# Performance work log

Hardware: AMD Instinct MI355X
Metric: run time of the kernel (lower is better)

The kernel has to match this reference:

```python
import jax, jax.numpy as jnp
import numpy as np

EPS = 1e-5

def _segment_mean(src_feat, edge_index, num_targets):
    # src_feat: [Ns, D]; edge_index: [2, E] = [source_idx, target_idx]
    msgs = src_feat[edge_index[0]]                                   # [E, D] gather
    agg = jax.ops.segment_sum(msgs, edge_index[1], num_segments=num_targets)
    deg = jax.ops.segment_sum(jnp.ones((edge_index.shape[1],), src_feat.dtype),
                              edge_index[1], num_segments=num_targets)
    return agg / jnp.clip(deg, 1.0)[:, None]

def _layernorm(x, gamma, beta):
    mu = jnp.mean(x, axis=-1, keepdims=True)
    var = jnp.mean(jnp.square(x - mu), axis=-1, keepdims=True)
    return (x - mu) * jax.lax.rsqrt(var + EPS) * gamma + beta

def setup_inputs() -> dict:
    key = jax.random.key(0)
    ks = jax.random.split(key, 8)
    NU, NI, E, D = 50000, 50000, 300000, 256
    s = 1.0 / np.sqrt(D)
    return {
        "user_features": jax.random.normal(ks[0], (NU, D), jnp.float32),
        "item_features": jax.random.normal(ks[1], (NI, D), jnp.float32),
        "user_item_edge_index": jax.random.randint(ks[2], (2, E), 0, NI),
        "item_user_edge_index": jax.random.randint(ks[3], (2, E), 0, NU),
        "Wu": jax.random.uniform(ks[4], (D, D), jnp.float32, -s, s),
        "bu": jax.random.uniform(ks[5], (D,), jnp.float32, -s, s),
        "Wi": jax.random.uniform(ks[6], (D, D), jnp.float32, -s, s),
        "bi": jax.random.uniform(ks[7], (D,), jnp.float32, -s, s),
        "gamma": jnp.ones((D,), jnp.float32),
        "beta": jnp.zeros((D,), jnp.float32),
    }

def reference(user_features, item_features, user_item_edge_index, item_user_edge_index,
              Wu, bu, Wi, bi, gamma, beta):
    num_items = item_features.shape[0]
    num_users = user_features.shape[0]
    # messages into items come from users; into users come from items
    item_messages = _segment_mean(user_features, user_item_edge_index, num_items)
    user_messages = _segment_mean(item_features, item_user_edge_index, num_users)
    u_new = (user_features + user_messages) @ Wu + bu
    i_new = (item_features + item_messages) @ Wi + bi
    u_new = _layernorm(jax.nn.relu(u_new), gamma, beta)
    i_new = _layernorm(jax.nn.relu(i_new), gamma, beta)
    return (u_new, i_new)
```

## Files before the change

kernel.cpp:

```cpp
#include <hip/hip_runtime.h>
#include <hip/hip_bf16.h>

#define D 256
#define BM 64
#define LDA 264
#define LDAF 260
#define LDK 72

typedef __attribute__((ext_vector_type(8))) __bf16 bf16x8;
typedef __attribute__((ext_vector_type(4))) float f32x4;

__device__ __forceinline__ float bf2f(unsigned short u) {
    union { unsigned int i; float f; } c; c.i = ((unsigned int)u) << 16; return c.f;
}
__device__ __forceinline__ float bf2f_lo(unsigned int u) {
    union { unsigned int i; float f; } c; c.i = u << 16; return c.f;
}
__device__ __forceinline__ float bf2f_hi(unsigned int u) {
    union { unsigned int i; float f; } c; c.i = u & 0xffff0000u; return c.f;
}
__device__ __forceinline__ unsigned short f2bf(float f) {
    __hip_bfloat16 h = __float2bfloat16(f);
    return *reinterpret_cast<unsigned short*>(&h);
}
__device__ __forceinline__ unsigned int pack2(float lo, float hi) {
    return (unsigned int)f2bf(lo) | ((unsigned int)f2bf(hi) << 16);
}


__global__ void k_prep(const float* __restrict__ uf, const float* __restrict__ itf,
                       const float* __restrict__ Wu, const float* __restrict__ Wi,
                       unsigned short* __restrict__ feat_bf,
                       unsigned short* __restrict__ Wt_u, unsigned short* __restrict__ Wt_i,
                       const int* __restrict__ iu_e, int Eiu,
                       const int* __restrict__ ui_e, int Eui,
                       int* __restrict__ deg, int NU,
                       size_t nfU, size_t nfTot, int nbF) {
    int b = blockIdx.x;
    if (b < nbF) {
        size_t base = ((size_t)b * 256 + threadIdx.x) * 8;
        if (base < nfTot) {
            const float* s = (base < nfU) ? (uf + base) : (itf + (base - nfU));
            float4 f0 = *(const float4*)s;
            float4 f1 = *(const float4*)(s + 4);
            ushort4 o0, o1;
            o0.x = f2bf(f0.x); o0.y = f2bf(f0.y); o0.z = f2bf(f0.z); o0.w = f2bf(f0.w);
            o1.x = f2bf(f1.x); o1.y = f2bf(f1.y); o1.z = f2bf(f1.z); o1.w = f2bf(f1.w);
            ((ushort4*)(feat_bf + base))[0] = o0;
            ((ushort4*)(feat_bf + base))[1] = o1;
        }
    } else if (b < nbF + 512) {
        int b2 = b - nbF;
        const float* W = (b2 < 256) ? Wu : Wi;
        unsigned short* Wt = (b2 < 256) ? Wt_u : Wt_i;
        int k = b2 & 255;
        int c = threadIdx.x;
        Wt[(size_t)c * 256 + k] = f2bf(W[(size_t)k * 256 + c]);
    } else {
        int e = (b - nbF - 512) * 256 + threadIdx.x;
        if (e < Eiu) {
            atomicAdd(&deg[iu_e[Eiu + e]], 1);
        } else if (e < Eiu + Eui) {
            int e2 = e - Eiu;
            atomicAdd(&deg[NU + ui_e[Eui + e2]], 1);
        }
    }
}

__global__ void k_scan_block(const int* __restrict__ deg, int N,
                             int* __restrict__ rs, int* __restrict__ bsums) {
    __shared__ int s[1024];
    int base = blockIdx.x * 1024;
    int t = threadIdx.x;
    int v = (base + t < N) ? deg[base + t] : 0;
    s[t] = v;
    __syncthreads();
    for (int off = 1; off < 1024; off <<= 1) {
        int add = (t >= off) ? s[t - off] : 0;
        __syncthreads();
        s[t] += add;
        __syncthreads();
    }
    if (base + t < N) rs[base + t + 1] = s[t];
    if (t == 1023) bsums[blockIdx.x] = s[1023];
}

__global__ void k_scan_sums(int* __restrict__ bsums, int nb) {
    __shared__ int s[1024];
    int t = threadIdx.x;
    int v = (t < nb) ? bsums[t] : 0;
    s[t] = v;
    __syncthreads();
    for (int off = 1; off < 1024; off <<= 1) {
        int add = (t >= off) ? s[t - off] : 0;
        __syncthreads();
        s[t] += add;
        __syncthreads();
    }
    if (t < nb) bsums[t] = s[t] - v;
}

__global__ void k_finalize(int N, int* __restrict__ rs, int* __restrict__ cur,
                           const int* __restrict__ bsums) {
    int i = blockIdx.x * blockDim.x + threadIdx.x;
    if (i < N) {
        int v = rs[i + 1] + bsums[i >> 10];
        rs[i + 1] = v;
        cur[i + 1] = v;
    }
    if (i == 0) { rs[0] = 0; cur[0] = 0; }
}

__global__ void k_fill2(const int* __restrict__ iu_e, int Eiu,
                        const int* __restrict__ ui_e, int Eui,
                        int* __restrict__ cur, int NU,
                        int* __restrict__ csr) {
    int e = blockIdx.x * blockDim.x + threadIdx.x;
    if (e < Eiu) {
        int d = iu_e[Eiu + e];
        int p = atomicAdd(&cur[d], 1);
        csr[p] = iu_e[e];
    } else if (e < Eiu + Eui) {
        int e2 = e - Eiu;
        int d = ui_e[Eui + e2];
        int p = atomicAdd(&cur[NU + d], 1);
        csr[p] = ui_e[e2];
    }
}

__global__ void k_msg2(const unsigned short* __restrict__ uf_bf,
                       const unsigned short* __restrict__ if_bf,
                       const int* __restrict__ rs, const int* __restrict__ csr,
                       unsigned short* __restrict__ x_u, unsigned short* __restrict__ x_i,
                       int NU, int NI) {
    int pair = (blockIdx.x * blockDim.x + threadIdx.x) >> 6;
    int lane = threadIdx.x & 63;
    int half = lane >> 5;
    int hl   = lane & 31;
    int Ntot = NU + NI;
    int wv = pair * 2 + half;
    if (wv >= Ntot) return;

    const unsigned short* src; const unsigned short* tgt; unsigned short* xo; int w;
    if (wv < NU) { src = if_bf; tgt = uf_bf; xo = x_u; w = wv; }
    else         { src = uf_bf; tgt = if_bf; xo = x_i; w = wv - NU; }

    int s0 = rs[wv], s1 = rs[wv + 1];
    float a0[8] = {}, a1[8] = {}, a2[8] = {}, a3[8] = {};

    int i = s0;
    for (; i + 4 <= s1; i += 4) {
        int e0 = csr[i], e1 = csr[i + 1], e2 = csr[i + 2], e3 = csr[i + 3];
        uint4 r0 = ((const uint4*)(src + (size_t)e0 * D))[hl];
        uint4 r1 = ((const uint4*)(src + (size_t)e1 * D))[hl];
        uint4 r2 = ((const uint4*)(src + (size_t)e2 * D))[hl];
        uint4 r3 = ((const uint4*)(src + (size_t)e3 * D))[hl];
        a0[0] += bf2f_lo(r0.x); a0[1] += bf2f_hi(r0.x); a0[2] += bf2f_lo(r0.y); a0[3] += bf2f_hi(r0.y);
        a0[4] += bf2f_lo(r0.z); a0[5] += bf2f_hi(r0.z); a0[6] += bf2f_lo(r0.w); a0[7] += bf2f_hi(r0.w);
        a1[0] += bf2f_lo(r1.x); a1[1] += bf2f_hi(r1.x); a1[2] += bf2f_lo(r1.y); a1[3] += bf2f_hi(r1.y);
        a1[4] += bf2f_lo(r1.z); a1[5] += bf2f_hi(r1.z); a1[6] += bf2f_lo(r1.w); a1[7] += bf2f_hi(r1.w);
        a2[0] += bf2f_lo(r2.x); a2[1] += bf2f_hi(r2.x); a2[2] += bf2f_lo(r2.y); a2[3] += bf2f_hi(r2.y);
        a2[4] += bf2f_lo(r2.z); a2[5] += bf2f_hi(r2.z); a2[6] += bf2f_lo(r2.w); a2[7] += bf2f_hi(r2.w);
        a3[0] += bf2f_lo(r3.x); a3[1] += bf2f_hi(r3.x); a3[2] += bf2f_lo(r3.y); a3[3] += bf2f_hi(r3.y);
        a3[4] += bf2f_lo(r3.z); a3[5] += bf2f_hi(r3.z); a3[6] += bf2f_lo(r3.w); a3[7] += bf2f_hi(r3.w);
    }
    for (; i < s1; ++i) {
        int e0 = csr[i];
        uint4 r0 = ((const uint4*)(src + (size_t)e0 * D))[hl];
        a0[0] += bf2f_lo(r0.x); a0[1] += bf2f_hi(r0.x); a0[2] += bf2f_lo(r0.y); a0[3] += bf2f_hi(r0.y);
        a0[4] += bf2f_lo(r0.z); a0[5] += bf2f_hi(r0.z); a0[6] += bf2f_lo(r0.w); a0[7] += bf2f_hi(r0.w);
    }

    int cnt = s1 - s0;
    float inv = 1.0f / (float)(cnt > 0 ? cnt : 1);
    uint4 tv = ((const uint4*)(tgt + (size_t)w * D))[hl];
    float x0 = bf2f_lo(tv.x) + (a0[0] + a1[0] + a2[0] + a3[0]) * inv;
    float x1 = bf2f_hi(tv.x) + (a0[1] + a1[1] + a2[1] + a3[1]) * inv;
    float x2 = bf2f_lo(tv.y) + (a0[2] + a1[2] + a2[2] + a3[2]) * inv;
    float x3 = bf2f_hi(tv.y) + (a0[3] + a1[3] + a2[3] + a3[3]) * inv;
    float x4 = bf2f_lo(tv.z) + (a0[4] + a1[4] + a2[4] + a3[4]) * inv;
    float x5 = bf2f_hi(tv.z) + (a0[5] + a1[5] + a2[5] + a3[5]) * inv;
    float x6 = bf2f_lo(tv.w) + (a0[6] + a1[6] + a2[6] + a3[6]) * inv;
    float x7 = bf2f_hi(tv.w) + (a0[7] + a1[7] + a2[7] + a3[7]) * inv;
    uint4 o;
    o.x = pack2(x0, x1); o.y = pack2(x2, x3); o.z = pack2(x4, x5); o.w = pack2(x6, x7);
    ((uint4*)(xo + (size_t)w * D))[hl] = o;
}

__launch_bounds__(256)
__global__ void k_gemm3(const unsigned short* __restrict__ x_u,
                        const unsigned short* __restrict__ x_i,
                        const unsigned short* __restrict__ Wt_u,
                        const unsigned short* __restrict__ Wt_i,
                        const float* __restrict__ bu, const float* __restrict__ bi,
                        const float* __restrict__ gamma, const float* __restrict__ beta,
                        int NU, int NI, int nbU, float* __restrict__ out) {
    __shared__ __align__(16) __hip_bfloat16 As[BM][LDA];
    __shared__ float red_s[BM][4];
    __shared__ float red_q[BM][4];

    int b = blockIdx.x;
    bool isU = b < nbU;
    const unsigned short* X  = isU ? x_u : x_i;
    const unsigned short* Wt = isU ? Wt_u : Wt_i;
    const float* bias        = isU ? bu : bi;
    float* Y                 = isU ? out : out + (size_t)NU * D;
    int N                    = isU ? NU : NI;
    int row0 = (isU ? b : b - nbU) * BM;

    int t = threadIdx.x;
    int lane = t & 63;
    int w = t >> 6;
    int l15 = lane & 15;
    int l4 = lane >> 4;

    {
        const uint4* Xg = (const uint4*)&X[(size_t)row0 * D];
        #pragma unroll
        for (int j = 0; j < 8; ++j) {
            int lr = (t >> 5) + j * 8;
            uint4 v = {0, 0, 0, 0};
            if (row0 + lr < N) v = Xg[(size_t)lr * 32 + (t & 31)];
            *(uint4*)&As[lr][(t & 31) * 8] = v;
        }
    }

    f32x4 acc[4][4];
    f32x4 zero = {0.f, 0.f, 0.f, 0.f};
    #pragma unroll
    for (int fr = 0; fr < 4; fr++)
        #pragma unroll
        for (int fc = 0; fc < 4; fc++)
            acc[fr][fc] = zero;

    __syncthreads();

    const uint4* Bg = (const uint4*)Wt;
    int colB = w * 64 + l15;
    #pragma unroll
    for (int ks8 = 0; ks8 < 8; ++ks8) {
        uint4 bq[4];
        #pragma unroll
        for (int fc = 0; fc < 4; ++fc)
            bq[fc] = Bg[(size_t)(colB + fc * 16) * 32 + ks8 * 4 + l4];
        bf16x8 af[4];
        #pragma unroll
        for (int fr = 0; fr < 4; ++fr)
            af[fr] = *(const bf16x8*)&As[fr * 16 + l15][ks8 * 32 + l4 * 8];
        #pragma unroll
        for (int fr = 0; fr < 4; ++fr)
            #pragma unroll
            for (int fc = 0; fc < 4; ++fc)
                acc[fr][fc] = __builtin_amdgcn_mfma_f32_16x16x32_bf16(
                    af[fr], *(bf16x8*)&bq[fc], acc[fr][fc], 0, 0, 0);
    }

    float bias_c[4], gam_c[4], bet_c[4];
    #pragma unroll
    for (int fc = 0; fc < 4; fc++) {
        int col = w * 64 + fc * 16 + l15;
        bias_c[fc] = bias[col];
        gam_c[fc]  = gamma[col];
        bet_c[fc]  = beta[col];
    }

    #pragma unroll
    for (int fr = 0; fr < 4; fr++) {
        #pragma unroll
        for (int r = 0; r < 4; r++) {
            int row = fr * 16 + l4 * 4 + r;
            float s = 0.f, q = 0.f;
            #pragma unroll
            for (int fc = 0; fc < 4; fc++) {
                float v = acc[fr][fc][r] + bias_c[fc];
                v = fmaxf(v, 0.f);
                acc[fr][fc][r] = v;
                s += v;
                q += v * v;
            }
            #pragma unroll
            for (int m = 1; m < 16; m <<= 1) {
                s += __shfl_xor(s, m);
                q += __shfl_xor(q, m);
            }
            if (l15 == 0) { red_s[row][w] = s; red_q[row][w] = q; }
        }
    }
    __syncthreads();

    float* AsF = (float*)&As[0][0];
    for (int h = 0; h < 2; ++h) {
        #pragma unroll
        for (int fr2 = 0; fr2 < 2; ++fr2) {
            int fr = h * 2 + fr2;
            #pragma unroll
            for (int r = 0; r < 4; ++r) {
                int row = fr * 16 + l4 * 4 + r;
                float s = red_s[row][0] + red_s[row][1] + red_s[row][2] + red_s[row][3];
                float q = red_q[row][0] + red_q[row][1] + red_q[row][2] + red_q[row][3];
                float mu  = s * (1.0f / 256.0f);
                float var = q * (1.0f / 256.0f) - mu * mu;
                float rstd = rsqrtf(var + 1e-5f);
                int lr = row - h * 32;
                #pragma unroll
                for (int fc = 0; fc < 4; ++fc) {
                    int col = w * 64 + fc * 16 + l15;
                    AsF[lr * LDAF + col] = (acc[fr][fc][r] - mu) * rstd * gam_c[fc] + bet_c[fc];
                }
            }
        }
        __syncthreads();
        #pragma unroll
        for (int j = 0; j < 8; ++j) {
            int r = j * 4 + w;
            int grow = row0 + h * 32 + r;
            if (grow < N) {
                float4 v = *(float4*)&AsF[r * LDAF + lane * 4];
                *(float4*)&Y[(size_t)grow * D + lane * 4] = v;
            }
        }
        __syncthreads();
    }
}


__global__ void k_hist(const int* __restrict__ dst, int E, int* __restrict__ deg) {
    int e = blockIdx.x * blockDim.x + threadIdx.x;
    if (e < E) atomicAdd(&deg[dst[e]], 1);
}

__global__ void k_finalize_rs(int N, int* __restrict__ rs, const int* __restrict__ bsums) {
    int i = blockIdx.x * blockDim.x + threadIdx.x;
    if (i < N) rs[i + 1] += bsums[i >> 10];
    if (i == 0) rs[0] = 0;
}

__global__ void k_fill(const int* __restrict__ src, const int* __restrict__ dst, int E,
                       const int* __restrict__ rs, int* __restrict__ cursor,
                       int* __restrict__ csr) {
    int e = blockIdx.x * blockDim.x + threadIdx.x;
    if (e < E) {
        int d = dst[e];
        int p = atomicAdd(&cursor[d], 1);
        csr[rs[d] + p] = src[e];
    }
}

__global__ void k_msg_x(const float* __restrict__ srcf, const float* __restrict__ tgtf,
                        const int* __restrict__ rs, const int* __restrict__ csr,
                        int N, float* __restrict__ xout) {
    int wave = (blockIdx.x * blockDim.x + threadIdx.x) >> 6;
    int lane = threadIdx.x & 63;
    if (wave >= N) return;
    int s0 = rs[wave], s1 = rs[wave + 1];
    float4 acc = make_float4(0.f, 0.f, 0.f, 0.f);
    for (int i = s0; i < s1; i++) {
        int s = csr[i];
        float4 f = *(const float4*)&srcf[(size_t)s * D + lane * 4];
        acc.x += f.x; acc.y += f.y; acc.z += f.z; acc.w += f.w;
    }
    int cnt = s1 - s0;
    float inv = 1.0f / (float)(cnt > 0 ? cnt : 1);
    float4 t = *(const float4*)&tgtf[(size_t)wave * D + lane * 4];
    float4 x;
    x.x = t.x + acc.x * inv;
    x.y = t.y + acc.y * inv;
    x.z = t.z + acc.z * inv;
    x.w = t.w + acc.w * inv;
    *(float4*)&xout[(size_t)wave * D + lane * 4] = x;
}

__global__ void k_wcvt(const float* __restrict__ W0, const float* __restrict__ W1,
                       __hip_bfloat16* __restrict__ Wt0, __hip_bfloat16* __restrict__ Wt1) {
    int b = blockIdx.x;
    const float* W = (b < 256) ? W0 : W1;
    __hip_bfloat16* Wt = (b < 256) ? Wt0 : Wt1;
    int k = b & 255;
    int c = threadIdx.x;
    Wt[(size_t)c * 256 + k] = __float2bfloat16(W[(size_t)k * 256 + c]);
}

__launch_bounds__(256)
__global__ void k_gemm_mfma_ln(const float* __restrict__ X,
                               const __hip_bfloat16* __restrict__ Wt,
                               const float* __restrict__ bias,
                               const float* __restrict__ gamma,
                               const float* __restrict__ beta,
                               int N, float* __restrict__ Y) {
    __shared__ __hip_bfloat16 As[BM][LDK];
    __shared__ __hip_bfloat16 Bs[D][LDK];
    __shared__ float red_s[BM][4];
    __shared__ float red_q[BM][4];

    int t = threadIdx.x;
    int lane = t & 63;
    int w = t >> 6;
    int l15 = lane & 15;
    int l4 = lane >> 4;
    int row0 = blockIdx.x * BM;

    f32x4 acc[4][4];
    f32x4 zero = {0.f, 0.f, 0.f, 0.f};
    #pragma unroll
    for (int fr = 0; fr < 4; fr++)
        #pragma unroll
        for (int fc = 0; fc < 4; fc++)
            acc[fr][fc] = zero;

    for (int k0 = 0; k0 < D; k0 += 64) {
        {
            int i = t >> 2;
            int kq = (t & 3) * 16;
            int r = row0 + i;
            float4 f[4];
            if (r < N) {
                const float4* p = (const float4*)&X[(size_t)r * D + k0 + kq];
                f[0] = p[0]; f[1] = p[1]; f[2] = p[2]; f[3] = p[3];
            } else {
                float4 z4 = make_float4(0.f, 0.f, 0.f, 0.f);
                f[0] = z4; f[1] = z4; f[2] = z4; f[3] = z4;
            }
            __hip_bfloat16 vb[16];
            #pragma unroll
            for (int q = 0; q < 4; q++) {
                vb[q * 4 + 0] = __float2bfloat16(f[q].x);
                vb[q * 4 + 1] = __float2bfloat16(f[q].y);
                vb[q * 4 + 2] = __float2bfloat16(f[q].z);
                vb[q * 4 + 3] = __float2bfloat16(f[q].w);
            }
            *(uint4*)&As[i][kq]     = *(uint4*)&vb[0];
            *(uint4*)&As[i][kq + 8] = *(uint4*)&vb[8];
        }
        #pragma unroll
        for (int pass = 0; pass < 4; pass++) {
            int c = pass * 64 + (t >> 2);
            int kq = (t & 3) * 16;
            const uint4* p = (const uint4*)&Wt[(size_t)c * D + k0 + kq];
            uint4 b0 = p[0], b1 = p[1];
            *(uint4*)&Bs[c][kq]     = b0;
            *(uint4*)&Bs[c][kq + 8] = b1;
        }
        __syncthreads();

        #pragma unroll
        for (int ks = 0; ks < 2; ks++) {
            bf16x8 af[4], bg[4];
            #pragma unroll
            for (int fr = 0; fr < 4; fr++)
                af[fr] = *(const bf16x8*)&As[fr * 16 + l15][ks * 32 + l4 * 8];
            #pragma unroll
            for (int fc = 0; fc < 4; fc++)
                bg[fc] = *(const bf16x8*)&Bs[w * 64 + fc * 16 + l15][ks * 32 + l4 * 8];
            #pragma unroll
            for (int fr = 0; fr < 4; fr++)
                #pragma unroll
                for (int fc = 0; fc < 4; fc++)
                    acc[fr][fc] = __builtin_amdgcn_mfma_f32_16x16x32_bf16(
                        af[fr], bg[fc], acc[fr][fc], 0, 0, 0);
        }
        __syncthreads();
    }

    float bias_c[4], gam_c[4], bet_c[4];
    #pragma unroll
    for (int fc = 0; fc < 4; fc++) {
        int col = w * 64 + fc * 16 + l15;
        bias_c[fc] = bias[col];
        gam_c[fc]  = gamma[col];
        bet_c[fc]  = beta[col];
    }

    #pragma unroll
    for (int fr = 0; fr < 4; fr++) {
        #pragma unroll
        for (int r = 0; r < 4; r++) {
            int row = fr * 16 + l4 * 4 + r;
            float s = 0.f, q = 0.f;
            #pragma unroll
            for (int fc = 0; fc < 4; fc++) {
                float v = acc[fr][fc][r] + bias_c[fc];
                v = fmaxf(v, 0.f);
                acc[fr][fc][r] = v;
                s += v;
                q += v * v;
            }
            #pragma unroll
            for (int m = 1; m < 16; m <<= 1) {
                s += __shfl_xor(s, m);
                q += __shfl_xor(q, m);
            }
            if (l15 == 0) { red_s[row][w] = s; red_q[row][w] = q; }
        }
    }
    __syncthreads();

    #pragma unroll
    for (int fr = 0; fr < 4; fr++) {
        #pragma unroll
        for (int r = 0; r < 4; r++) {
            int row = fr * 16 + l4 * 4 + r;
            int grow = row0 + row;
            if (grow >= N) continue;
            float s = red_s[row][0] + red_s[row][1] + red_s[row][2] + red_s[row][3];
            float q = red_q[row][0] + red_q[row][1] + red_q[row][2] + red_q[row][3];
            float mu  = s * (1.0f / 256.0f);
            float var = q * (1.0f / 256.0f) - mu * mu;
            float rstd = rsqrtf(var + 1e-5f);
            #pragma unroll
            for (int fc = 0; fc < 4; fc++) {
                int col = w * 64 + fc * 16 + l15;
                Y[(size_t)grow * D + col] = (acc[fr][fc][r] - mu) * rstd * gam_c[fc] + bet_c[fc];
            }
        }
    }
}


extern "C" void kernel_launch(void* const* d_in, const int* in_sizes, int n_in,
                              void* d_out, int out_size, void* d_ws, size_t ws_size,
                              hipStream_t stream) {
    const float* uf    = (const float*)d_in[0];
    const float* itf   = (const float*)d_in[1];
    const int*   ui_e  = (const int*)d_in[2];
    const int*   iu_e  = (const int*)d_in[3];
    const float* Wu    = (const float*)d_in[4];
    const float* bu    = (const float*)d_in[5];
    const float* Wi    = (const float*)d_in[6];
    const float* bi    = (const float*)d_in[7];
    const float* gamma = (const float*)d_in[8];
    const float* beta  = (const float*)d_in[9];

    int NU  = in_sizes[0] / D;
    int NI  = in_sizes[1] / D;
    int Eui = in_sizes[2] / 2;
    int Eiu = in_sizes[3] / 2;
    int Nmax = NU > NI ? NU : NI;
    int Ntot = NU + NI;
    int Etot = Eiu + Eui;

    float* out   = (float*)d_out;
    size_t nfU = (size_t)NU * D;
    size_t nfI = (size_t)NI * D;
    size_t nfTot = nfU + nfI;

    unsigned short* uf_bf = (unsigned short*)d_ws;
    unsigned short* if_bf = uf_bf + nfU;
    unsigned short* x_u   = if_bf + nfI;
    unsigned short* x_i   = x_u + nfU;
    unsigned short* Wt_u2 = x_i + nfI;
    unsigned short* Wt_i2 = Wt_u2 + 65536;
    int* deg2  = (int*)(Wt_i2 + 65536);
    int* rs2   = deg2 + Ntot;
    int* cur2  = rs2 + Ntot + 1;
    int* bsums = cur2 + Ntot + 1;
    int* csr2  = bsums + 1024;
    size_t needed = (size_t)((char*)(csr2 + Etot) - (char*)d_ws);

    if (ws_size >= needed) {
        int nbF = (int)((nfTot + 2047) / 2048);
        int nbH = (Etot + 255) / 256;
        hipMemsetAsync(deg2, 0, (size_t)Ntot * sizeof(int), stream);
        k_prep<<<nbF + 512 + nbH, 256, 0, stream>>>(uf, itf, Wu, Wi, uf_bf, Wt_u2, Wt_i2,
                                                    iu_e, Eiu, ui_e, Eui, deg2, NU,
                                                    nfU, nfTot, nbF);
        int nb = (Ntot + 1023) / 1024;
        k_scan_block<<<nb, 1024, 0, stream>>>(deg2, Ntot, rs2, bsums);
        k_scan_sums<<<1, 1024, 0, stream>>>(bsums, nb);
        k_finalize<<<(Ntot + 255) / 256, 256, 0, stream>>>(Ntot, rs2, cur2, bsums);
        k_fill2<<<nbH, 256, 0, stream>>>(iu_e, Eiu, ui_e, Eui, cur2, NU, csr2);
        int pairs = (Ntot + 1) / 2;
        k_msg2<<<(pairs + 3) / 4, 256, 0, stream>>>(uf_bf, if_bf, rs2, csr2, x_u, x_i, NU, NI);
        int nbU = (NU + BM - 1) / BM;
        int nbI = (NI + BM - 1) / BM;
        k_gemm3<<<nbU + nbI, 256, 0, stream>>>(x_u, x_i, Wt_u2, Wt_i2, bu, bi, gamma, beta,
                                               NU, NI, nbU, out);
        return;
    }

    float* u_out = out;
    float* i_out = out + nfU;
    __hip_bfloat16* Wt_u = (__hip_bfloat16*)d_ws;
    __hip_bfloat16* Wt_i = Wt_u + 256 * 256;
    int* deg    = (int*)(Wt_i + 256 * 256);
    int* rs     = deg + Nmax;
    int* bs     = rs + Nmax + 1;
    int* cursor = bs + 1024;
    int* csr    = cursor + Nmax;

    k_wcvt<<<512, 256, 0, stream>>>(Wu, Wi, Wt_u, Wt_i);

    auto run_side = [&](const float* srcf, const float* tgtf, const int* edges, int E,
                        int N, const __hip_bfloat16* Wt, const float* bias, float* y) {
        const int* esrc = edges;
        const int* edst = edges + E;
        hipMemsetAsync(deg, 0, (size_t)N * sizeof(int), stream);
        hipMemsetAsync(cursor, 0, (size_t)N * sizeof(int), stream);
        k_hist<<<(E + 255) / 256, 256, 0, stream>>>(edst, E, deg);
        int nb = (N + 1023) / 1024;
        k_scan_block<<<nb, 1024, 0, stream>>>(deg, N, rs, bs);
        k_scan_sums<<<1, 1024, 0, stream>>>(bs, nb);
        k_finalize_rs<<<(N + 255) / 256, 256, 0, stream>>>(N, rs, bs);
        k_fill<<<(E + 255) / 256, 256, 0, stream>>>(esrc, edst, E, rs, cursor, csr);
        k_msg_x<<<(N + 3) / 4, 256, 0, stream>>>(srcf, tgtf, rs, csr, N, y);
        k_gemm_mfma_ln<<<(N + BM - 1) / BM, 256, 0, stream>>>(y, Wt, bias, gamma, beta, N, y);
    };

    run_side(itf, uf, iu_e, Eiu, NU, Wt_u, bu, u_out);
    run_side(uf, itf, ui_e, Eui, NI, Wt_i, bi, i_out);
}
```

Before: 226.3 us.

## Halve GEMM row tile to 32 and store LayerNorm output directly to global

The fused GEMM+ReLU+LayerNorm kernel now processes 32 rows per block instead of 64. That halves accumulator registers and LDS use and doubles the block count. The epilogue drops the LDS-staged transpose and its two barriers per half, and each lane writes its normalized values straight to global memory. The trade-offs are strided 4-byte scattered stores instead of coalesced float4 writes, and twice as many reloads of the weight matrix per output row.

```diff
diff --git a/kernel.cpp b/kernel.cpp
--- a/kernel.cpp
+++ b/kernel.cpp
@@ -3,8 +3,8 @@
 
 #define D 256
 #define BM 64
+#define BM2 32
 #define LDA 264
-#define LDAF 260
 #define LDK 72
 
 typedef __attribute__((ext_vector_type(8))) __bf16 bf16x8;
@@ -188,16 +188,16 @@
 }
 
 __launch_bounds__(256)
-__global__ void k_gemm3(const unsigned short* __restrict__ x_u,
+__global__ void k_gemm5(const unsigned short* __restrict__ x_u,
                         const unsigned short* __restrict__ x_i,
                         const unsigned short* __restrict__ Wt_u,
                         const unsigned short* __restrict__ Wt_i,
                         const float* __restrict__ bu, const float* __restrict__ bi,
                         const float* __restrict__ gamma, const float* __restrict__ beta,
                         int NU, int NI, int nbU, float* __restrict__ out) {
-    __shared__ __align__(16) __hip_bfloat16 As[BM][LDA];
-    __shared__ float red_s[BM][4];
-    __shared__ float red_q[BM][4];
+    __shared__ __align__(16) __hip_bfloat16 As[BM2][LDA];
+    __shared__ float red_s[BM2][4];
+    __shared__ float red_q[BM2][4];
 
     int b = blockIdx.x;
     bool isU = b < nbU;
@@ -206,7 +206,7 @@
     const float* bias        = isU ? bu : bi;
     float* Y                 = isU ? out : out + (size_t)NU * D;
     int N                    = isU ? NU : NI;
-    int row0 = (isU ? b : b - nbU) * BM;
+    int row0 = (isU ? b : b - nbU) * BM2;
 
     int t = threadIdx.x;
     int lane = t & 63;
@@ -217,18 +217,20 @@
     {
         const uint4* Xg = (const uint4*)&X[(size_t)row0 * D];
         #pragma unroll
-        for (int j = 0; j < 8; ++j) {
-            int lr = (t >> 5) + j * 8;
+        for (int j = 0; j < 4; ++j) {
+            int f = j * 256 + t;
+            int lr = f >> 5;
+            int c = f & 31;
             uint4 v = {0, 0, 0, 0};
-            if (row0 + lr < N) v = Xg[(size_t)lr * 32 + (t & 31)];
-            *(uint4*)&As[lr][(t & 31) * 8] = v;
-        }
-    }
-
-    f32x4 acc[4][4];
+            if (row0 + lr < N) v = Xg[(size_t)lr * 32 + c];
+            *(uint4*)&As[lr][c * 8] = v;
+        }
+    }
+
+    f32x4 acc[2][4];
     f32x4 zero = {0.f, 0.f, 0.f, 0.f};
     #pragma unroll
-    for (int fr = 0; fr < 4; fr++)
+    for (int fr = 0; fr < 2; fr++)
         #pragma unroll
         for (int fc = 0; fc < 4; fc++)
             acc[fr][fc] = zero;
@@ -243,12 +245,12 @@
         #pragma unroll
         for (int fc = 0; fc < 4; ++fc)
             bq[fc] = Bg[(size_t)(colB + fc * 16) * 32 + ks8 * 4 + l4];
-        bf16x8 af[4];
-        #pragma unroll
-        for (int fr = 0; fr < 4; ++fr)
+        bf16x8 af[2];
+        #pragma unroll
+        for (int fr = 0; fr < 2; ++fr)
             af[fr] = *(const bf16x8*)&As[fr * 16 + l15][ks8 * 32 + l4 * 8];
         #pragma unroll
-        for (int fr = 0; fr < 4; ++fr)
+        for (int fr = 0; fr < 2; ++fr)
             #pragma unroll
             for (int fc = 0; fc < 4; ++fc)
                 acc[fr][fc] = __builtin_amdgcn_mfma_f32_16x16x32_bf16(
@@ -265,7 +267,7 @@
     }
 
     #pragma unroll
-    for (int fr = 0; fr < 4; fr++) {
+    for (int fr = 0; fr < 2; fr++) {
         #pragma unroll
         for (int r = 0; r < 4; r++) {
             int row = fr * 16 + l4 * 4 + r;
@@ -288,38 +290,24 @@
     }
     __syncthreads();
 
-    float* AsF = (float*)&As[0][0];
-    for (int h = 0; h < 2; ++h) {
-        #pragma unroll
-        for (int fr2 = 0; fr2 < 2; ++fr2) {
-            int fr = h * 2 + fr2;
-            #pragma unroll
-            for (int r = 0; r < 4; ++r) {
-                int row = fr * 16 + l4 * 4 + r;
-                float s = red_s[row][0] + red_s[row][1] + red_s[row][2] + red_s[row][3];
-                float q = red_q[row][0] + red_q[row][1] + red_q[row][2] + red_q[row][3];
-                float mu  = s * (1.0f / 256.0f);
-                float var = q * (1.0f / 256.0f) - mu * mu;
-                float rstd = rsqrtf(var + 1e-5f);
-                int lr = row - h * 32;
-                #pragma unroll
-                for (int fc = 0; fc < 4; ++fc) {
-                    int col = w * 64 + fc * 16 + l15;
-                    AsF[lr * LDAF + col] = (acc[fr][fc][r] - mu) * rstd * gam_c[fc] + bet_c[fc];
-                }
-            }
-        }
-        __syncthreads();
-        #pragma unroll
-        for (int j = 0; j < 8; ++j) {
-            int r = j * 4 + w;
-            int grow = row0 + h * 32 + r;
-            if (grow < N) {
-                float4 v = *(float4*)&AsF[r * LDAF + lane * 4];
-                *(float4*)&Y[(size_t)grow * D + lane * 4] = v;
-            }
-        }
-        __syncthreads();
+    #pragma unroll
+    for (int fr = 0; fr < 2; fr++) {
+        #pragma unroll
+        for (int r = 0; r < 4; r++) {
+            int row = fr * 16 + l4 * 4 + r;
+            int grow = row0 + row;
+            if (grow >= N) continue;
+            float s = red_s[row][0] + red_s[row][1] + red_s[row][2] + red_s[row][3];
+            float q = red_q[row][0] + red_q[row][1] + red_q[row][2] + red_q[row][3];
+            float mu  = s * (1.0f / 256.0f);
+            float var = q * (1.0f / 256.0f) - mu * mu;
+            float rstd = rsqrtf(var + 1e-5f);
+            #pragma unroll
+            for (int fc = 0; fc < 4; fc++) {
+                int col = w * 64 + fc * 16 + l15;
+                Y[(size_t)grow * D + col] = (acc[fr][fc][r] - mu) * rstd * gam_c[fc] + bet_c[fc];
+            }
+        }
     }
 }
 
@@ -570,9 +558,9 @@
         k_fill2<<<nbH, 256, 0, stream>>>(iu_e, Eiu, ui_e, Eui, cur2, NU, csr2);
         int pairs = (Ntot + 1) / 2;
         k_msg2<<<(pairs + 3) / 4, 256, 0, stream>>>(uf_bf, if_bf, rs2, csr2, x_u, x_i, NU, NI);
-        int nbU = (NU + BM - 1) / BM;
-        int nbI = (NI + BM - 1) / BM;
-        k_gemm3<<<nbU + nbI, 256, 0, stream>>>(x_u, x_i, Wt_u2, Wt_i2, bu, bi, gamma, beta,
+        int nbU = (NU + BM2 - 1) / BM2;
+        int nbI = (NI + BM2 - 1) / BM2;
+        k_gemm5<<<nbU + nbI, 256, 0, stream>>>(x_u, x_i, Wt_u2, Wt_i2, bu, bi, gamma, beta,
                                                NU, NI, nbU, out);
         return;
     }
```

Measured after the change: 218.0 us (median of 2 runs). 1.04x faster.
